# Kernel tuning notes

Measured on AMD Instinct MI355X. Metric: run time of the kernel, lower is better.

The kernel has to match this reference:

```python
import jax, jax.numpy as jnp
import numpy as np

B, F, E, C = 2048, 39, 64, 64  # batch, num_fields, embed_dim, conv_size


def setup_inputs() -> dict:
    key = jax.random.key(0)
    k1, k2, k3 = jax.random.split(key, 3)
    x_emb = jax.random.normal(k1, (B, F, E), dtype=jnp.float32)
    # Conv2d(1, C, (2, E), (2, 1)) weight: (C, 1, 2, E), bias: (C,)
    W = jax.random.normal(k2, (C, 1, 2, E), dtype=jnp.float32) * 0.05
    b = jax.random.normal(k3, (C,), dtype=jnp.float32) * 0.05
    return {"x_emb": x_emb, "W": W, "b": b}


def reference(x_emb, W, b):
    Bn, Fn, En = x_emb.shape
    # All C(F,2) ordered pairs (i<j), same order as the python double loop
    ii, jj = np.triu_indices(Fn, k=1)  # each length P
    xi = x_emb[:, ii]  # (B, P, E)
    xj = x_emb[:, jj]  # (B, P, E)
    # kernel (2, E) with stride (2, 1) over the stacked (2P, E) map is a
    # shared linear over each pair: y[b,p,c] = xi.Wi[c] + xj.Wj[c] + bias[c]
    Wi = W[:, 0, 0, :]  # (C, E)
    Wj = W[:, 0, 1, :]  # (C, E)
    y = jnp.einsum('bpe,ce->bpc', xi, Wi) + jnp.einsum('bpe,ce->bpc', xj, Wj) + b
    y = jax.nn.relu(y)  # (B, P, C)
    # torch conv output is (B, C, P, 1) contiguous; .view(B, -1, C) reshapes
    # that C-major buffer into (B, P, C) WITHOUT transposing -> replicate exactly
    Cn = y.shape[-1]
    out = jnp.transpose(y, (0, 2, 1)).reshape(Bn, -1, Cn)
    return out
```

## Files before the change

### kernel.cpp

```cpp
#include <hip/hip_runtime.h>


#define BATCH 2048
#define FDIM  39
#define EDIM  64
#define CDIM  64
#define NPAIR 741
#define XSTR  40
#define WSTR  132
#define ASTR  41

__global__ __launch_bounds__(256) void interconv_fused(
    const float* __restrict__ x,
    const float* __restrict__ Wg,
    const float* __restrict__ bias,
    float* __restrict__ out)
{
    __shared__ float smem[EDIM * XSTR + EDIM * WSTR];
    __shared__ int   tab[NPAIR];
    __shared__ float sbias[CDIM];

    float* xT = smem;
    float* Wl = smem + EDIM * XSTR;
    float* A  = smem;

    const int tid = threadIdx.x;
    const int b   = blockIdx.x;
    const float* xg = x + (size_t)b * (FDIM * EDIM);

    for (int q = tid; q < (FDIM * EDIM) / 4; q += 256) {
        float4 v = ((const float4*)xg)[q];
        int flat = q << 2;
        int f  = flat >> 6;
        int e0 = flat & 63;
        xT[(e0 + 0) * XSTR + f] = v.x;
        xT[(e0 + 1) * XSTR + f] = v.y;
        xT[(e0 + 2) * XSTR + f] = v.z;
        xT[(e0 + 3) * XSTR + f] = v.w;
    }
    for (int q = tid; q < (CDIM * 2 * EDIM) / 4; q += 256) {
        float4 v = ((const float4*)Wg)[q];
        int flat = q << 2;
        int c   = flat >> 7;
        int rem = flat & 127;
        int wh  = rem >> 6;
        int e0  = rem & 63;
        int cw  = (wh << 6) | c;
        Wl[(e0 + 0) * WSTR + cw] = v.x;
        Wl[(e0 + 1) * WSTR + cw] = v.y;
        Wl[(e0 + 2) * WSTR + cw] = v.z;
        Wl[(e0 + 3) * WSTR + cw] = v.w;
    }
    for (int idx = tid; idx < NPAIR; idx += 256) {
        int i = (int)floorf((77.0f - sqrtf(5929.0f - 8.0f * (float)idx)) * 0.5f);
        i = i < 0 ? 0 : (i > FDIM - 2 ? FDIM - 2 : i);
        while ((i + 1) * (77 - (i + 1)) / 2 <= idx) ++i;
        while (i * (77 - i) / 2 > idx) --i;
        int j = idx - i * (77 - i) / 2 + i + 1;
        tab[idx] = i | (j << 8);
    }
    if (tid < CDIM) sbias[tid] = bias[tid];
    __syncthreads();

    const int ft  = tid >> 5;
    const int ct  = tid & 31;
    const int f0  = ft * 5;
    const int cw0 = ct * 4;

    float acc[5][4];
#pragma unroll
    for (int a = 0; a < 5; ++a)
#pragma unroll
        for (int q = 0; q < 4; ++q) acc[a][q] = 0.0f;

#pragma unroll 4
    for (int e = 0; e < EDIM; ++e) {
        float4 wv = *(const float4*)(Wl + e * WSTR + cw0);
        float xv[5];
#pragma unroll
        for (int a = 0; a < 5; ++a) xv[a] = xT[e * XSTR + f0 + a];
#pragma unroll
        for (int a = 0; a < 5; ++a) {
            acc[a][0] = fmaf(xv[a], wv.x, acc[a][0]);
            acc[a][1] = fmaf(xv[a], wv.y, acc[a][1]);
            acc[a][2] = fmaf(xv[a], wv.z, acc[a][2]);
            acc[a][3] = fmaf(xv[a], wv.w, acc[a][3]);
        }
    }
    __syncthreads();

#pragma unroll
    for (int a = 0; a < 5; ++a)
#pragma unroll
        for (int q = 0; q < 4; ++q)
            A[(cw0 + q) * ASTR + (f0 + a)] = acc[a][q];
    __syncthreads();

    float* outb = out + (size_t)b * (CDIM * NPAIR);
    for (int c = 0; c < CDIM; ++c) {
        const float bc = sbias[c];
        const float* rI = A + c * ASTR;
        const float* rJ = A + (64 + c) * ASTR;
        float* oc = outb + c * NPAIR;
        for (int p = tid; p < NPAIR; p += 256) {
            int t = tab[p];
            float v = rI[t & 0xff] + rJ[t >> 8] + bc;
            oc[p] = v > 0.0f ? v : 0.0f;
        }
    }
}

extern "C" void kernel_launch(void* const* d_in, const int* in_sizes, int n_in,
                              void* d_out, int out_size, void* d_ws, size_t ws_size,
                              hipStream_t stream) {
    const float* x    = (const float*)d_in[0];
    const float* W    = (const float*)d_in[1];
    const float* bias = (const float*)d_in[2];
    float* out        = (float*)d_out;

    interconv_fused<<<dim3(BATCH), dim3(256), 0, stream>>>(x, W, bias, out);
}
```

Measured before the change: 434.8 us.

## Transpose shared A to field-major and vectorize epilogue with nontemporal stores

Stores the per-field projection buffer A field-major (stride 132), so each thread reads float4 rows for its fixed pair across channels instead of scalar gathers per channel. Pair indices are precomputed once per thread from the table, which removes the per-channel table lookups. Output writes use nontemporal stores to avoid polluting cache with the large write stream. Risks include LDS bank conflicts on the float4 reads from varying field rows and higher register pressure from the unrolled epilogue.

```diff
diff --git a/kernel.cpp b/kernel.cpp
--- a/kernel.cpp
+++ b/kernel.cpp
@@ -6,9 +6,10 @@
 #define EDIM  64
 #define CDIM  64
 #define NPAIR 741
+#define CP    (CDIM * NPAIR)
 #define XSTR  40
 #define WSTR  132
-#define ASTR  41
+#define ASTR  132
 
 __global__ __launch_bounds__(256) void interconv_fused(
     const float* __restrict__ x,
@@ -62,10 +63,19 @@
     if (tid < CDIM) sbias[tid] = bias[tid];
     __syncthreads();
 
+    int iOff[3], jOff[3];
+#pragma unroll
+    for (int k = 0; k < 3; ++k) {
+        int p = tid + (k << 8);
+        int t = (p < NPAIR) ? tab[p] : 0;
+        iOff[k] = (t & 0xff) * ASTR;
+        jOff[k] = (t >> 8) * ASTR + CDIM;
+    }
+
     const int ft  = tid >> 5;
     const int ct  = tid & 31;
     const int f0  = ft * 5;
-    const int cw0 = ct * 4;
+    const int cw0 = ct << 2;
 
     float acc[5][4];
 #pragma unroll
@@ -90,22 +100,33 @@
     __syncthreads();
 
 #pragma unroll
-    for (int a = 0; a < 5; ++a)
-#pragma unroll
-        for (int q = 0; q < 4; ++q)
-            A[(cw0 + q) * ASTR + (f0 + a)] = acc[a][q];
+    for (int a = 0; a < 5; ++a) {
+        float4 v = make_float4(acc[a][0], acc[a][1], acc[a][2], acc[a][3]);
+        *(float4*)(A + (f0 + a) * ASTR + cw0) = v;
+    }
     __syncthreads();
 
-    float* outb = out + (size_t)b * (CDIM * NPAIR);
-    for (int c = 0; c < CDIM; ++c) {
-        const float bc = sbias[c];
-        const float* rI = A + c * ASTR;
-        const float* rJ = A + (64 + c) * ASTR;
-        float* oc = outb + c * NPAIR;
-        for (int p = tid; p < NPAIR; p += 256) {
-            int t = tab[p];
-            float v = rI[t & 0xff] + rJ[t >> 8] + bc;
-            oc[p] = v > 0.0f ? v : 0.0f;
+    float* outb = out + (size_t)b * CP;
+#pragma unroll
+    for (int k = 0; k < 3; ++k) {
+        if (k == 2 && tid >= NPAIR - 512) continue;
+        const int p = tid + (k << 8);
+        const float* aI = A + iOff[k];
+        const float* aJ = A + jOff[k];
+        float* op = outb + p;
+#pragma unroll
+        for (int cq = 0; cq < 16; ++cq) {
+            float4 vi = *(const float4*)(aI + (cq << 2));
+            float4 vj = *(const float4*)(aJ + (cq << 2));
+            float4 bb = *(const float4*)(sbias + (cq << 2));
+            float r0 = vi.x + vj.x + bb.x; r0 = r0 > 0.0f ? r0 : 0.0f;
+            float r1 = vi.y + vj.y + bb.y; r1 = r1 > 0.0f ? r1 : 0.0f;
+            float r2 = vi.z + vj.z + bb.z; r2 = r2 > 0.0f ? r2 : 0.0f;
+            float r3 = vi.w + vj.w + bb.w; r3 = r3 > 0.0f ? r3 : 0.0f;
+            __builtin_nontemporal_store(r0, op + (cq * 4 + 0) * NPAIR);
+            __builtin_nontemporal_store(r1, op + (cq * 4 + 1) * NPAIR);
+            __builtin_nontemporal_store(r2, op + (cq * 4 + 2) * NPAIR);
+            __builtin_nontemporal_store(r3, op + (cq * 4 + 3) * NPAIR);
         }
     }
 }
```

Result: slower. 490.3 us (+12.8%).

## Split fused kernel into row GEMM plus pair-gather kernel via workspace

Applied to the files above, without the earlier changes.

Splits the single per-batch kernel into two launches. The first is a GEMM over all batch×field rows, 32 rows per block, that writes per-field projections to a workspace. The second is a gather kernel that reads those projections into LDS, computes pair indices in registers instead of a table, and writes the ReLU outputs with fixed per-thread pair slots. This aims to raise GEMM efficiency and simplify the store loop, at the cost of an extra global round trip for the workspace (about 40 MB) and a second launch. The old fused kernel is kept as a fallback when the workspace is too small.

```diff
diff --git a/kernel.cpp b/kernel.cpp
--- a/kernel.cpp
+++ b/kernel.cpp
@@ -6,9 +6,122 @@
 #define EDIM  64
 #define CDIM  64
 #define NPAIR 741
+#define CP    (CDIM * NPAIR)
+#define NROWS (BATCH * FDIM)
+#define WSTR  132
+#define ASTR2 129
+#define AWSBYTES ((size_t)NROWS * 128 * 4)
+
+__global__ __launch_bounds__(256) void interconv_gemm(
+    const float* __restrict__ x,
+    const float* __restrict__ Wg,
+    float* __restrict__ Ag)
+{
+    __shared__ float xL[32 * EDIM];
+    __shared__ float Wl[EDIM * WSTR];
+
+    const int tid = threadIdx.x;
+    const size_t rowBase = (size_t)blockIdx.x * 32;
+    const float* xg = x + rowBase * EDIM;
+
+    for (int q = tid; q < 512; q += 256)
+        ((float4*)xL)[q] = ((const float4*)xg)[q];
+    for (int q = tid; q < 2048; q += 256) {
+        float4 v = ((const float4*)Wg)[q];
+        int flat = q << 2;
+        int c   = flat >> 7;
+        int rem = flat & 127;
+        int wh  = rem >> 6;
+        int e0  = rem & 63;
+        int cw  = (wh << 6) | c;
+        Wl[(e0 + 0) * WSTR + cw] = v.x;
+        Wl[(e0 + 1) * WSTR + cw] = v.y;
+        Wl[(e0 + 2) * WSTR + cw] = v.z;
+        Wl[(e0 + 3) * WSTR + cw] = v.w;
+    }
+    __syncthreads();
+
+    const int cg  = tid & 31;
+    const int rg  = tid >> 5;
+    const int cw0 = cg << 2;
+    const int r0  = rg << 2;
+
+    float acc[4][4];
+#pragma unroll
+    for (int a = 0; a < 4; ++a)
+#pragma unroll
+        for (int q = 0; q < 4; ++q) acc[a][q] = 0.0f;
+
+#pragma unroll 4
+    for (int e = 0; e < EDIM; ++e) {
+        float4 wv = *(const float4*)(Wl + e * WSTR + cw0);
+        float xv[4];
+#pragma unroll
+        for (int a = 0; a < 4; ++a) xv[a] = xL[(r0 + a) * EDIM + e];
+#pragma unroll
+        for (int a = 0; a < 4; ++a) {
+            acc[a][0] = fmaf(xv[a], wv.x, acc[a][0]);
+            acc[a][1] = fmaf(xv[a], wv.y, acc[a][1]);
+            acc[a][2] = fmaf(xv[a], wv.z, acc[a][2]);
+            acc[a][3] = fmaf(xv[a], wv.w, acc[a][3]);
+        }
+    }
+
+    float* Aout = Ag + (rowBase + r0) * 128 + cw0;
+#pragma unroll
+    for (int a = 0; a < 4; ++a)
+        *(float4*)(Aout + a * 128) = make_float4(acc[a][0], acc[a][1], acc[a][2], acc[a][3]);
+}
+
+__global__ __launch_bounds__(256) void interconv_gather(
+    const float* __restrict__ Ag,
+    const float* __restrict__ bias,
+    float* __restrict__ out)
+{
+    __shared__ float As[FDIM * ASTR2];
+    __shared__ float sbias[CDIM];
+
+    const int tid = threadIdx.x;
+    const int b   = blockIdx.x;
+    const float* Ab = Ag + (size_t)b * (FDIM * 128);
+
+    for (int q = tid; q < FDIM * 128; q += 256)
+        As[(q >> 7) * ASTR2 + (q & 127)] = Ab[q];
+    if (tid < CDIM) sbias[tid] = bias[tid];
+    __syncthreads();
+
+    int iB[3], jB[3];
+#pragma unroll
+    for (int k = 0; k < 3; ++k) {
+        int p = tid + (k << 8);
+        if (p >= NPAIR) p = 0;
+        int i = (int)floorf((77.0f - sqrtf(5929.0f - 8.0f * (float)p)) * 0.5f);
+        i = i < 0 ? 0 : (i > FDIM - 2 ? FDIM - 2 : i);
+        while ((i + 1) * (77 - (i + 1)) / 2 <= p) ++i;
+        while (i * (77 - i) / 2 > p) --i;
+        int j = p - i * (77 - i) / 2 + i + 1;
+        iB[k] = i * ASTR2;
+        jB[k] = j * ASTR2 + CDIM;
+    }
+
+    float* outb = out + (size_t)b * CP;
+    const bool full3 = (tid < NPAIR - 512);
+
+#pragma unroll 4
+    for (int c = 0; c < CDIM; ++c) {
+        const float bc = sbias[c];
+        float v0 = As[iB[0] + c] + As[jB[0] + c] + bc;
+        float v1 = As[iB[1] + c] + As[jB[1] + c] + bc;
+        float v2 = As[iB[2] + c] + As[jB[2] + c] + bc;
+        float* oc = outb + c * NPAIR + tid;
+        oc[0]   = v0 > 0.0f ? v0 : 0.0f;
+        oc[256] = v1 > 0.0f ? v1 : 0.0f;
+        if (full3) oc[512] = v2 > 0.0f ? v2 : 0.0f;
+    }
+}
+
 #define XSTR  40
-#define WSTR  132
-#define ASTR  41
+#define ASTRF 41
 
 __global__ __launch_bounds__(256) void interconv_fused(
     const float* __restrict__ x,
@@ -65,7 +178,7 @@
     const int ft  = tid >> 5;
     const int ct  = tid & 31;
     const int f0  = ft * 5;
-    const int cw0 = ct * 4;
+    const int cw0 = ct << 2;
 
     float acc[5][4];
 #pragma unroll
@@ -93,14 +206,14 @@
     for (int a = 0; a < 5; ++a)
 #pragma unroll
         for (int q = 0; q < 4; ++q)
-            A[(cw0 + q) * ASTR + (f0 + a)] = acc[a][q];
-    __syncthreads();
-
-    float* outb = out + (size_t)b * (CDIM * NPAIR);
+            A[(cw0 + q) * ASTRF + (f0 + a)] = acc[a][q];
+    __syncthreads();
+
+    float* outb = out + (size_t)b * CP;
     for (int c = 0; c < CDIM; ++c) {
         const float bc = sbias[c];
-        const float* rI = A + c * ASTR;
-        const float* rJ = A + (64 + c) * ASTR;
+        const float* rI = A + c * ASTRF;
+        const float* rJ = A + (64 + c) * ASTRF;
         float* oc = outb + c * NPAIR;
         for (int p = tid; p < NPAIR; p += 256) {
             int t = tab[p];
@@ -118,5 +231,11 @@
     const float* bias = (const float*)d_in[2];
     float* out        = (float*)d_out;
 
-    interconv_fused<<<dim3(BATCH), dim3(256), 0, stream>>>(x, W, bias, out);
-}
+    if (ws_size >= AWSBYTES) {
+        float* Ag = (float*)d_ws;
+        interconv_gemm<<<dim3(NROWS / 32), dim3(256), 0, stream>>>(x, W, Ag);
+        interconv_gather<<<dim3(BATCH), dim3(256), 0, stream>>>(Ag, bias, out);
+    } else {
+        interconv_fused<<<dim3(BATCH), dim3(256), 0, stream>>>(x, W, bias, out);
+    }
+}
```

Measured after the change: 452.0 us. +4.0%, slower.
